# Performance work log

Hardware: AMD Instinct MI355X
Metric: run time of the kernel (lower is better)

Reference implementation:

```python
import jax, jax.numpy as jnp
import numpy as np

EPS = 1e-5
SLOPE = 0.2


def _bn(x, g, b, m, v):
    # eval-mode BatchNorm1d over channel dim (last axis here)
    return (x - m) * (g * jax.lax.rsqrt(v + EPS)) + b


def _lrelu(x):
    return jnp.where(x >= 0, x, SLOPE * x)


def setup_inputs() -> dict:
    key = jax.random.key(0)
    ks = jax.random.split(key, 24)
    B, N = 16, 2048
    d = {
        "x_query": jax.random.normal(ks[0], (B, 2048), jnp.float32),
        "x_key": jax.random.normal(ks[1], (B, N, 512), jnp.float32),
        "W1": jax.random.normal(ks[2], (2048, 512), jnp.float32) * 0.02,
        "W2": jax.random.normal(ks[3], (512, 2048), jnp.float32) * 0.02,
        "W3": jax.random.normal(ks[4], (64, 512), jnp.float32) * 0.02,
        "W4": jax.random.normal(ks[5], (1, 64), jnp.float32) * 0.02,
    }
    for i, c in zip(range(4), (2048, 512, 64, 1)):
        d[f"g{i+1}"] = jax.random.uniform(ks[6 + 4 * i], (c,), jnp.float32, 0.5, 1.5)
        d[f"b{i+1}"] = jax.random.normal(ks[7 + 4 * i], (c,), jnp.float32) * 0.1
        d[f"m{i+1}"] = jax.random.normal(ks[8 + 4 * i], (c,), jnp.float32) * 0.1
        d[f"v{i+1}"] = jax.random.uniform(ks[9 + 4 * i], (c,), jnp.float32, 0.5, 1.5)
    return d


def reference(x_query, x_key, W1, W2, W3, W4,
              g1, b1, m1, v1, g2, b2, m2, v2,
              g3, b3, m3, v3, g4, b4, m4, v4):
    # values: [B, N, 2048]
    values = _lrelu(_bn(jnp.einsum('bnd,ed->bne', x_key, W1), g1, b1, m1, v1))
    features = values + x_query[:, None, :]
    s = _lrelu(_bn(jnp.einsum('bne,de->bnd', features, W2), g2, b2, m2, v2))
    s = _lrelu(_bn(jnp.einsum('bnd,kd->bnk', s, W3), g3, b3, m3, v3))
    s = _lrelu(_bn(jnp.einsum('bnk,ok->bno', s, W4), g4, b4, m4, v4))  # [B,N,1]
    scores = jax.nn.softmax(s[..., 0], axis=1)  # [B,N]
    feature = jnp.einsum('bne,bn->be', values, scores)  # softmax-weighted sum pool
    return feature
```

## Files before the change

kernel.cpp:

```cpp
#include <hip/hip_runtime.h>
#include <hip/hip_bf16.h>

typedef __bf16 bf16x8 __attribute__((ext_vector_type(8)));
typedef float f32x4 __attribute__((ext_vector_type(4)));
typedef __attribute__((address_space(3))) void lds_void_t;
typedef __attribute__((address_space(1))) void gbl_void_t;

#define LRELU(x) ((x) >= 0.f ? (x) : 0.2f * (x))

__device__ __forceinline__ void gload16(void* lds_uniform, const void* gsrc) {
    __builtin_amdgcn_global_load_lds((const gbl_void_t*)gsrc, (lds_void_t*)lds_uniform,
                                     16, 0, 0);
}

__device__ __forceinline__ unsigned short f2u(float f) {
    __hip_bfloat16 h = __float2bfloat16(f);
    return reinterpret_cast<unsigned short&>(h);
}

__global__ void cvt_fused(const float* __restrict__ a, __hip_bfloat16* __restrict__ oa, int na,
                          const float* __restrict__ b, __hip_bfloat16* __restrict__ ob, int nb,
                          const float* __restrict__ c, __hip_bfloat16* __restrict__ oc, int nc,
                          const float* __restrict__ d, __hip_bfloat16* __restrict__ od, int nd) {
    const int stride = gridDim.x * blockDim.x;
    const int total = na + nb + nc + nd;
    for (int i = blockIdx.x * blockDim.x + threadIdx.x; i < total; i += stride) {
        const float* s; __hip_bfloat16* o; int j = i;
        if (j < na) { s = a; o = oa; }
        else {
            j -= na;
            if (j < nb) { s = b; o = ob; }
            else {
                j -= nb;
                if (j < nc) { s = c; o = oc; }
                else { j -= nc; s = d; o = od; }
            }
        }
        float4 v = reinterpret_cast<const float4*>(s)[j];
        ushort4 u;
        u.x = f2u(v.x); u.y = f2u(v.y); u.z = f2u(v.z); u.w = f2u(v.w);
        reinterpret_cast<ushort4*>(o)[j] = u;
    }
}


#define MMQ(AF, BF, IH, JH)                                                   \
    {                                                                         \
        _Pragma("unroll") for (int r = 0; r < 4; ++r) {                       \
            _Pragma("unroll") for (int c = 0; c < 2; ++c) {                   \
                _Pragma("unroll") for (int s = 0; s < 2; ++s) {               \
                    acc[(IH) * 4 + r][(JH) * 2 + c] =                         \
                        __builtin_amdgcn_mfma_f32_16x16x32_bf16(              \
                            AF[r][s], BF[c][s],                               \
                            acc[(IH) * 4 + r][(JH) * 2 + c], 0, 0, 0);        \
                }                                                             \
            }                                                                 \
        }                                                                     \
    }

#define LDA_(AF, BUF, IH)                                                     \
    {                                                                         \
        const __hip_bfloat16* _ab = sm + (BUF) * 32768 + wm * 8192;           \
        _Pragma("unroll") for (int r = 0; r < 4; ++r) {                       \
            const int _row = (IH) * 64 + r * 16 + lr;                         \
            _Pragma("unroll") for (int s = 0; s < 2; ++s) {                   \
                AF[r][s] = *reinterpret_cast<const bf16x8*>(                  \
                    _ab + _row * 64 + (((s * 4 + kg) ^ (lr & 7)) * 8));       \
            }                                                                 \
        }                                                                     \
    }

#define LDB_(BF, BUF, JH)                                                     \
    {                                                                         \
        const __hip_bfloat16* _bb =                                           \
            sm + (BUF) * 32768 + (2 + (wn >> 1)) * 8192;                      \
        _Pragma("unroll") for (int c = 0; c < 2; ++c) {                       \
            const int _row = (wn & 1) * 64 + ((JH) * 2 + c) * 16 + lr;        \
            _Pragma("unroll") for (int s = 0; s < 2; ++s) {                   \
                BF[c][s] = *reinterpret_cast<const bf16x8*>(                  \
                    _bb + _row * 64 + (((s * 4 + kg) ^ (lr & 7)) * 8));       \
            }                                                                 \
        }                                                                     \
    }

#define PH_MID                                                                \
    __builtin_amdgcn_s_barrier();                                             \
    asm volatile("s_waitcnt lgkmcnt(0)" ::: "memory");                        \
    __builtin_amdgcn_sched_barrier(0);                                        \
    __builtin_amdgcn_s_setprio(1);

#define PH_END                                                                \
    __builtin_amdgcn_s_setprio(0);                                            \
    __builtin_amdgcn_sched_barrier(0);                                        \
    __builtin_amdgcn_s_barrier();

template <int N, int K, int MODE>
__global__ __launch_bounds__(512, 1)
void gemm8p(const __hip_bfloat16* __restrict__ A,
            const __hip_bfloat16* __restrict__ Bw,
            const float* __restrict__ xq,
            __hip_bfloat16* __restrict__ out,
            const float* __restrict__ Gg, const float* __restrict__ Gb,
            const float* __restrict__ Gm, const float* __restrict__ Gv) {
    __shared__ __hip_bfloat16 sm[65536];

    const int nwg = gridDim.x;
    const int cpx = nwg >> 3;
    const int bid = blockIdx.x;
    const int orig = (bid & 7) * cpx + (bid >> 3);
    constexpr int NCB = N / 256;
    const int row0 = (orig / NCB) * 256;
    const int col0 = (orig % NCB) * 256;

    const int tid = threadIdx.x;
    const int lane = tid & 63;
    const int wv = tid >> 6;
    const int wm = wv >> 2, wn = wv & 3;
    const int lr = lane & 15, kg = lane >> 4;

    const int schunk = (tid & 7) ^ ((tid >> 3) & 7);
    const __hip_bfloat16* srcA0 = A + (size_t)(row0 + (tid >> 3)) * K + schunk * 8;
    const __hip_bfloat16* srcB0 = Bw + (size_t)(col0 + (tid >> 3)) * K + schunk * 8;
    constexpr size_t H = (size_t)128 * K;

    auto STG = [&](int buf, int region, const __hip_bfloat16* src) {
        __hip_bfloat16* l = sm + buf * 32768 + region * 8192 + wv * 512;
        gload16(l, src);
        gload16(l + 4096, src + (size_t)64 * K);
    };

    f32x4 acc[8][4];
#pragma unroll
    for (int i = 0; i < 8; ++i)
#pragma unroll
        for (int j = 0; j < 4; ++j) acc[i][j] = (f32x4){0.f, 0.f, 0.f, 0.f};

    bf16x8 af[4][2], bfrL[2][2], bfrH[2][2];

    STG(0, 0, srcA0);
    STG(0, 1, srcA0 + H);
    STG(0, 2, srcB0);
    STG(0, 3, srcB0 + H);
    STG(1, 2, srcB0 + 64);
    STG(1, 3, srcB0 + H + 64);
    asm volatile("s_waitcnt vmcnt(4)" ::: "memory");
    __builtin_amdgcn_s_barrier();

    constexpr int niter = K / 128;
    for (int it = 0; it < niter; ++it) {
        const int k0 = it * 128;
        const bool pf = (it + 1 < niter);

        LDA_(af, 0, 0);
        LDB_(bfrL, 0, 0);
        STG(1, 0, srcA0 + k0 + 64);
        PH_MID; MMQ(af, bfrL, 0, 0); PH_END;

        LDB_(bfrH, 0, 1);
        STG(1, 1, srcA0 + H + k0 + 64);
        PH_MID; MMQ(af, bfrH, 0, 1); PH_END;

        LDA_(af, 0, 1);
        if (pf) STG(0, 2, srcB0 + k0 + 128);
        PH_MID; MMQ(af, bfrH, 1, 1); PH_END;

        if (pf) {
            STG(0, 3, srcB0 + H + k0 + 128);
            asm volatile("s_waitcnt vmcnt(4)" ::: "memory");
        } else {
            asm volatile("s_waitcnt vmcnt(0)" ::: "memory");
        }
        PH_MID; MMQ(af, bfrL, 1, 0); PH_END;

        LDA_(af, 1, 0);
        LDB_(bfrL, 1, 0);
        if (pf) STG(0, 0, srcA0 + k0 + 128);
        PH_MID; MMQ(af, bfrL, 0, 0); PH_END;

        LDB_(bfrH, 1, 1);
        if (pf) STG(0, 1, srcA0 + H + k0 + 128);
        PH_MID; MMQ(af, bfrH, 0, 1); PH_END;

        LDA_(af, 1, 1);
        if (pf) STG(1, 2, srcB0 + k0 + 192);
        PH_MID; MMQ(af, bfrH, 1, 1); PH_END;

        if (pf) {
            STG(1, 3, srcB0 + H + k0 + 192);
            asm volatile("s_waitcnt vmcnt(4)" ::: "memory");
        } else {
            asm volatile("s_waitcnt vmcnt(0)" ::: "memory");
        }
        PH_MID; MMQ(af, bfrL, 1, 0); PH_END;
    }

    const int bq = row0 >> 11;
    float scl[4], tcn[4], xqv[4];
#pragma unroll
    for (int j = 0; j < 4; ++j) {
        const int c = col0 + wn * 64 + j * 16 + lr;
        scl[j] = Gg[c] * rsqrtf(Gv[c] + 1e-5f);
        tcn[j] = Gb[c] - Gm[c] * scl[j];
        xqv[j] = (MODE == 1) ? xq[bq * 2048 + c] : 0.f;
    }
#pragma unroll
    for (int i = 0; i < 8; ++i) {
#pragma unroll
        for (int rI = 0; rI < 4; ++rI) {
            const int r = row0 + wm * 128 + i * 16 + kg * 4 + rI;
            const size_t rowoff = (size_t)r * N + col0 + wn * 64 + lr;
#pragma unroll
            for (int j = 0; j < 4; ++j) {
                float val = acc[i][j][rI] * scl[j] + tcn[j];
                val = LRELU(val) + xqv[j];
                out[rowoff + j * 16] = __float2bfloat16(val);
            }
        }
    }
}

__global__ __launch_bounds__(256, 2)
void gemm3_l4(const __hip_bfloat16* __restrict__ A,
              const __hip_bfloat16* __restrict__ W3b,
              const float* __restrict__ W4,
              const float* __restrict__ g3, const float* __restrict__ b3,
              const float* __restrict__ m3, const float* __restrict__ v3,
              const float* __restrict__ g4, const float* __restrict__ b4,
              const float* __restrict__ m4, const float* __restrict__ v4,
              float* __restrict__ logits) {
    __shared__ __hip_bfloat16 lA[128 * 32];
    __shared__ __hip_bfloat16 lB[64 * 520];
    const int tid = threadIdx.x;
    const int lane = tid & 63;
    const int wv = tid >> 6;
    const int row0 = blockIdx.x * 128;
    const int lr = lane & 15, kg = lane >> 4;

#pragma unroll
    for (int p = 0; p < 16; ++p) {
        const int idx = tid * 8 + p * 2048;
        const int r = idx >> 9, c = idx & 511;
        bf16x8 v = *reinterpret_cast<const bf16x8*>(W3b + idx);
        *reinterpret_cast<bf16x8*>(&lB[r * 520 + c]) = v;
    }

    const int schunk = (lane & 3) ^ ((lane >> 3) & 3);
    const __hip_bfloat16* Ag = A + (size_t)(row0 + wv * 32 + (lane >> 2)) * 512 + schunk * 8;
    __hip_bfloat16* lAp = lA + wv * 1024;

    const int koff = ((kg ^ ((lr >> 1) & 3)) << 3);
    const int aoff = (wv * 32 + lr) * 32 + koff;

    f32x4 acc[2][4];
#pragma unroll
    for (int i = 0; i < 2; ++i)
#pragma unroll
        for (int j = 0; j < 4; ++j) acc[i][j] = (f32x4){0.f, 0.f, 0.f, 0.f};

    for (int k = 0; k < 512; k += 32) {
        gload16(lAp,       Ag + k);
        gload16(lAp + 512, Ag + k + (size_t)16 * 512);
        __syncthreads();

        bf16x8 a[2], b[4];
#pragma unroll
        for (int i = 0; i < 2; ++i)
            a[i] = *reinterpret_cast<const bf16x8*>(lA + aoff + i * 512);
#pragma unroll
        for (int j = 0; j < 4; ++j)
            b[j] = *reinterpret_cast<const bf16x8*>(&lB[(j * 16 + lr) * 520 + k + kg * 8]);
#pragma unroll
        for (int i = 0; i < 2; ++i)
#pragma unroll
            for (int j = 0; j < 4; ++j)
                acc[i][j] = __builtin_amdgcn_mfma_f32_16x16x32_bf16(a[i], b[j], acc[i][j], 0, 0, 0);
        __syncthreads();
    }

    const float sc4 = g4[0] * rsqrtf(v4[0] + 1e-5f);
    const float tc4 = b4[0] - m4[0] * sc4;
#pragma unroll
    for (int i = 0; i < 2; ++i) {
        float t[4] = {0.f, 0.f, 0.f, 0.f};
#pragma unroll
        for (int j = 0; j < 4; ++j) {
            const int c = j * 16 + lr;
            const float sc = g3[c] * rsqrtf(v3[c] + 1e-5f);
            const float tc = b3[c] - m3[c] * sc;
            const float w4c = W4[c];
#pragma unroll
            for (int rI = 0; rI < 4; ++rI) {
                float v = acc[i][j][rI] * sc + tc;
                t[rI] += LRELU(v) * w4c;
            }
        }
#pragma unroll
        for (int m = 1; m < 16; m <<= 1)
#pragma unroll
            for (int rI = 0; rI < 4; ++rI) t[rI] += __shfl_xor(t[rI], m, 64);
        if (lr == 0) {
#pragma unroll
            for (int rI = 0; rI < 4; ++rI) {
                float lg = t[rI] * sc4 + tc4;
                logits[row0 + wv * 32 + i * 16 + kg * 4 + rI] = LRELU(lg);
            }
        }
    }
}

__global__ void softmax2048(const float* __restrict__ logits, float* __restrict__ scores) {
    __shared__ float sh[2048];
    __shared__ float red[256];
    const int b = blockIdx.x, tid = threadIdx.x;
    float lmax = -1e30f;
#pragma unroll
    for (int it = 0; it < 8; ++it) {
        const int n = tid + it * 256;
        float v = logits[b * 2048 + n];
        sh[n] = v;
        lmax = fmaxf(lmax, v);
    }
    red[tid] = lmax;
    __syncthreads();
    for (int s = 128; s > 0; s >>= 1) {
        if (tid < s) red[tid] = fmaxf(red[tid], red[tid + s]);
        __syncthreads();
    }
    const float gmax = red[0];
    __syncthreads();
    float lsum = 0.f;
#pragma unroll
    for (int it = 0; it < 8; ++it) {
        const int n = tid + it * 256;
        float e = expf(sh[n] - gmax);
        sh[n] = e;
        lsum += e;
    }
    red[tid] = lsum;
    __syncthreads();
    for (int s = 128; s > 0; s >>= 1) {
        if (tid < s) red[tid] += red[tid + s];
        __syncthreads();
    }
    const float inv = 1.f / red[0];
#pragma unroll
    for (int it = 0; it < 8; ++it) {
        const int n = tid + it * 256;
        scores[b * 2048 + n] = sh[n] * inv;
    }
}

__global__ void pool_partial(const __hip_bfloat16* __restrict__ feats,
                             const float* __restrict__ scores,
                             float* __restrict__ partial) {
    const int b = blockIdx.y, nc = blockIdx.x;
    const int e0 = threadIdx.x * 8;
    float acc[8] = {0, 0, 0, 0, 0, 0, 0, 0};
    const size_t base = ((size_t)b * 2048 + nc * 64) * 2048;
    for (int i = 0; i < 64; ++i) {
        const float sc = scores[b * 2048 + nc * 64 + i];
        bf16x8 v = *reinterpret_cast<const bf16x8*>(feats + base + (size_t)i * 2048 + e0);
#pragma unroll
        for (int j = 0; j < 8; ++j) acc[j] += sc * (float)v[j];
    }
    float* p = partial + ((size_t)(b * 32 + nc)) * 2048 + e0;
#pragma unroll
    for (int j = 0; j < 8; ++j) p[j] = acc[j];
}

__global__ void pool_reduce(const float* __restrict__ partial,
                            const float* __restrict__ xq,
                            float* __restrict__ out) {
    const int i = blockIdx.x * blockDim.x + threadIdx.x;
    const int b = i >> 11, e = i & 2047;
    float s = 0.f;
#pragma unroll
    for (int nc = 0; nc < 32; ++nc) s += partial[((size_t)(b * 32 + nc)) * 2048 + e];
    out[i] = s - xq[i];
}

extern "C" void kernel_launch(void* const* d_in, const int* in_sizes, int n_in,
                              void* d_out, int out_size, void* d_ws, size_t ws_size,
                              hipStream_t stream) {
    const float* xq = (const float*)d_in[0];
    const float* xk = (const float*)d_in[1];
    const float* W1 = (const float*)d_in[2];
    const float* W2 = (const float*)d_in[3];
    const float* W3 = (const float*)d_in[4];
    const float* W4 = (const float*)d_in[5];
    const float* g1 = (const float*)d_in[6], *b1 = (const float*)d_in[7];
    const float* m1 = (const float*)d_in[8], *v1 = (const float*)d_in[9];
    const float* g2 = (const float*)d_in[10], *b2 = (const float*)d_in[11];
    const float* m2 = (const float*)d_in[12], *v2 = (const float*)d_in[13];
    const float* g3 = (const float*)d_in[14], *b3 = (const float*)d_in[15];
    const float* m3 = (const float*)d_in[16], *v3 = (const float*)d_in[17];
    const float* g4 = (const float*)d_in[18], *b4 = (const float*)d_in[19];
    const float* m4 = (const float*)d_in[20], *v4 = (const float*)d_in[21];

    const int M = 32768;

    char* ws = (char*)d_ws;
    size_t off = 0;
    auto alloc = [&](size_t bytes) {
        void* p = ws + off;
        off += (bytes + 255) & ~(size_t)255;
        return p;
    };
    __hip_bfloat16* xkb   = (__hip_bfloat16*)alloc((size_t)M * 512 * 2);
    __hip_bfloat16* w1b   = (__hip_bfloat16*)alloc((size_t)2048 * 512 * 2);
    __hip_bfloat16* w2b   = (__hip_bfloat16*)alloc((size_t)512 * 2048 * 2);
    __hip_bfloat16* w3b   = (__hip_bfloat16*)alloc((size_t)64 * 512 * 2);
    __hip_bfloat16* featb = (__hip_bfloat16*)alloc((size_t)M * 2048 * 2);
    __hip_bfloat16* s2b   = (__hip_bfloat16*)alloc((size_t)M * 512 * 2);
    float* logits         = (float*)alloc((size_t)M * 4);
    float* scores         = (float*)alloc((size_t)16 * 2048 * 4);
    float* partial        = (float*)alloc((size_t)16 * 32 * 2048 * 4);

    cvt_fused<<<4096, 256, 0, stream>>>(
        xk, xkb, M * 512 / 4,
        W1, w1b, 2048 * 512 / 4,
        W2, w2b, 512 * 2048 / 4,
        W3, w3b, 64 * 512 / 4);

    gemm8p<2048, 512, 1><<<1024, 512, 0, stream>>>(
        xkb, w1b, xq, featb, g1, b1, m1, v1);

    gemm8p<512, 2048, 2><<<256, 512, 0, stream>>>(
        featb, w2b, nullptr, s2b, g2, b2, m2, v2);

    gemm3_l4<<<256, 256, 0, stream>>>(s2b, w3b, W4,
                                      g3, b3, m3, v3, g4, b4, m4, v4, logits);

    softmax2048<<<16, 256, 0, stream>>>(logits, scores);

    pool_partial<<<dim3(32, 16), 256, 0, stream>>>(featb, scores, partial);
    pool_reduce<<<128, 256, 0, stream>>>(partial, xq, (float*)d_out);
}
```

Measured before the change: 205.1 us.

## Fuse x_key fp32-to-bf16 conversion into first GEMM's A-tile loader

Drops the separate pass that converted x_key (32768x512 fp32) to a bf16 buffer. The first GEMM now reads fp32 A tiles straight into registers, converts them to bf16 and writes them to LDS, with register double-buffering woven into the existing pipelined schedule. This removes a full read and write of the converted activation buffer. In exchange the first GEMM reads twice as many bytes for A, uses more VGPRs, and loses async direct-to-LDS loads for A.

```diff
diff --git a/kernel.cpp b/kernel.cpp
--- a/kernel.cpp
+++ b/kernel.cpp
@@ -18,23 +18,18 @@
     return reinterpret_cast<unsigned short&>(h);
 }
 
-__global__ void cvt_fused(const float* __restrict__ a, __hip_bfloat16* __restrict__ oa, int na,
-                          const float* __restrict__ b, __hip_bfloat16* __restrict__ ob, int nb,
-                          const float* __restrict__ c, __hip_bfloat16* __restrict__ oc, int nc,
-                          const float* __restrict__ d, __hip_bfloat16* __restrict__ od, int nd) {
+__global__ void cvt_w(const float* __restrict__ a, __hip_bfloat16* __restrict__ oa, int na,
+                      const float* __restrict__ b, __hip_bfloat16* __restrict__ ob, int nb,
+                      const float* __restrict__ c, __hip_bfloat16* __restrict__ oc, int nc) {
     const int stride = gridDim.x * blockDim.x;
-    const int total = na + nb + nc + nd;
+    const int total = na + nb + nc;
     for (int i = blockIdx.x * blockDim.x + threadIdx.x; i < total; i += stride) {
         const float* s; __hip_bfloat16* o; int j = i;
         if (j < na) { s = a; o = oa; }
         else {
             j -= na;
             if (j < nb) { s = b; o = ob; }
-            else {
-                j -= nb;
-                if (j < nc) { s = c; o = oc; }
-                else { j -= nc; s = d; o = od; }
-            }
+            else { j -= nb; s = c; o = oc; }
         }
         float4 v = reinterpret_cast<const float4*>(s)[j];
         ushort4 u;
@@ -94,9 +89,10 @@
     __builtin_amdgcn_sched_barrier(0);                                        \
     __builtin_amdgcn_s_barrier();
 
-template <int N, int K, int MODE>
+template <int N, int K, int MODE, int ASRC>
 __global__ __launch_bounds__(512, 1)
 void gemm8p(const __hip_bfloat16* __restrict__ A,
+            const float* __restrict__ Af,
             const __hip_bfloat16* __restrict__ Bw,
             const float* __restrict__ xq,
             __hip_bfloat16* __restrict__ out,
@@ -120,6 +116,7 @@
 
     const int schunk = (tid & 7) ^ ((tid >> 3) & 7);
     const __hip_bfloat16* srcA0 = A + (size_t)(row0 + (tid >> 3)) * K + schunk * 8;
+    const float* srcAf = Af + (size_t)(row0 + (tid >> 3)) * K + schunk * 8;
     const __hip_bfloat16* srcB0 = Bw + (size_t)(col0 + (tid >> 3)) * K + schunk * 8;
     constexpr size_t H = (size_t)128 * K;
 
@@ -128,6 +125,26 @@
         gload16(l, src);
         gload16(l + 4096, src + (size_t)64 * K);
     };
+    auto LD_A32 = [&](float4* r, int elemoff) {
+#pragma unroll
+        for (int g = 0; g < 2; ++g) {
+            const float* s = srcAf + elemoff + g * (size_t)64 * K;
+            r[g * 2 + 0] = *reinterpret_cast<const float4*>(s);
+            r[g * 2 + 1] = *reinterpret_cast<const float4*>(s + 4);
+        }
+    };
+    auto WR_A32 = [&](int buf, int region, const float4* r) {
+        __hip_bfloat16* l = sm + buf * 32768 + region * 8192 + tid * 8;
+#pragma unroll
+        for (int g = 0; g < 2; ++g) {
+            bf16x8 v;
+            v[0] = (__bf16)r[g * 2].x;     v[1] = (__bf16)r[g * 2].y;
+            v[2] = (__bf16)r[g * 2].z;     v[3] = (__bf16)r[g * 2].w;
+            v[4] = (__bf16)r[g * 2 + 1].x; v[5] = (__bf16)r[g * 2 + 1].y;
+            v[6] = (__bf16)r[g * 2 + 1].z; v[7] = (__bf16)r[g * 2 + 1].w;
+            *reinterpret_cast<bf16x8*>(l + g * 4096) = v;
+        }
+    };
 
     f32x4 acc[8][4];
 #pragma unroll
@@ -136,14 +153,28 @@
         for (int j = 0; j < 4; ++j) acc[i][j] = (f32x4){0.f, 0.f, 0.f, 0.f};
 
     bf16x8 af[4][2], bfrL[2][2], bfrH[2][2];
-
-    STG(0, 0, srcA0);
-    STG(0, 1, srcA0 + H);
-    STG(0, 2, srcB0);
-    STG(0, 3, srcB0 + H);
-    STG(1, 2, srcB0 + 64);
-    STG(1, 3, srcB0 + H + 64);
-    asm volatile("s_waitcnt vmcnt(4)" ::: "memory");
+    float4 rE0[4], rE1[4], rO0[4], rO1[4];
+
+    if constexpr (ASRC == 1) {
+        float4 t0[4], t1[4];
+        LD_A32(t0, 0); LD_A32(t1, (int)H);
+        STG(0, 2, srcB0);
+        STG(0, 3, srcB0 + H);
+        STG(1, 2, srcB0 + 64);
+        STG(1, 3, srcB0 + H + 64);
+        LD_A32(rO0, 64); LD_A32(rO1, (int)H + 64);
+        WR_A32(0, 0, t0); WR_A32(0, 1, t1);
+        asm volatile("s_waitcnt vmcnt(12)" ::: "memory");
+        asm volatile("s_waitcnt lgkmcnt(0)" ::: "memory");
+    } else {
+        STG(0, 0, srcA0);
+        STG(0, 1, srcA0 + H);
+        STG(0, 2, srcB0);
+        STG(0, 3, srcB0 + H);
+        STG(1, 2, srcB0 + 64);
+        STG(1, 3, srcB0 + H + 64);
+        asm volatile("s_waitcnt vmcnt(4)" ::: "memory");
+    }
     __builtin_amdgcn_s_barrier();
 
     constexpr int niter = K / 128;
@@ -151,13 +182,23 @@
         const int k0 = it * 128;
         const bool pf = (it + 1 < niter);
 
+        if constexpr (ASRC == 1) {
+            if (pf) LD_A32(rE0, k0 + 128);
+            WR_A32(1, 0, rO0);
+        } else {
+            STG(1, 0, srcA0 + k0 + 64);
+        }
         LDA_(af, 0, 0);
         LDB_(bfrL, 0, 0);
-        STG(1, 0, srcA0 + k0 + 64);
         PH_MID; MMQ(af, bfrL, 0, 0); PH_END;
 
+        if constexpr (ASRC == 1) {
+            if (pf) LD_A32(rE1, (int)H + k0 + 128);
+            WR_A32(1, 1, rO1);
+        } else {
+            STG(1, 1, srcA0 + H + k0 + 64);
+        }
         LDB_(bfrH, 0, 1);
-        STG(1, 1, srcA0 + H + k0 + 64);
         PH_MID; MMQ(af, bfrH, 0, 1); PH_END;
 
         LDA_(af, 0, 1);
@@ -166,7 +207,10 @@
 
         if (pf) {
             STG(0, 3, srcB0 + H + k0 + 128);
-            asm volatile("s_waitcnt vmcnt(4)" ::: "memory");
+            if constexpr (ASRC == 1)
+                asm volatile("s_waitcnt vmcnt(12)" ::: "memory");
+            else
+                asm volatile("s_waitcnt vmcnt(4)" ::: "memory");
         } else {
             asm volatile("s_waitcnt vmcnt(0)" ::: "memory");
         }
@@ -174,11 +218,19 @@
 
         LDA_(af, 1, 0);
         LDB_(bfrL, 1, 0);
-        if (pf) STG(0, 0, srcA0 + k0 + 128);
+        if constexpr (ASRC == 1) {
+            if (pf) { LD_A32(rO0, k0 + 192); WR_A32(0, 0, rE0); }
+        } else {
+            if (pf) STG(0, 0, srcA0 + k0 + 128);
+        }
         PH_MID; MMQ(af, bfrL, 0, 0); PH_END;
 
         LDB_(bfrH, 1, 1);
-        if (pf) STG(0, 1, srcA0 + H + k0 + 128);
+        if constexpr (ASRC == 1) {
+            if (pf) { LD_A32(rO1, (int)H + k0 + 192); WR_A32(0, 1, rE1); }
+        } else {
+            if (pf) STG(0, 1, srcA0 + H + k0 + 128);
+        }
         PH_MID; MMQ(af, bfrH, 0, 1); PH_END;
 
         LDA_(af, 1, 1);
@@ -187,7 +239,10 @@
 
         if (pf) {
             STG(1, 3, srcB0 + H + k0 + 192);
-            asm volatile("s_waitcnt vmcnt(4)" ::: "memory");
+            if constexpr (ASRC == 1)
+                asm volatile("s_waitcnt vmcnt(12)" ::: "memory");
+            else
+                asm volatile("s_waitcnt vmcnt(4)" ::: "memory");
         } else {
             asm volatile("s_waitcnt vmcnt(0)" ::: "memory");
         }
@@ -406,7 +461,6 @@
         off += (bytes + 255) & ~(size_t)255;
         return p;
     };
-    __hip_bfloat16* xkb   = (__hip_bfloat16*)alloc((size_t)M * 512 * 2);
     __hip_bfloat16* w1b   = (__hip_bfloat16*)alloc((size_t)2048 * 512 * 2);
     __hip_bfloat16* w2b   = (__hip_bfloat16*)alloc((size_t)512 * 2048 * 2);
     __hip_bfloat16* w3b   = (__hip_bfloat16*)alloc((size_t)64 * 512 * 2);
@@ -416,17 +470,16 @@
     float* scores         = (float*)alloc((size_t)16 * 2048 * 4);
     float* partial        = (float*)alloc((size_t)16 * 32 * 2048 * 4);
 
-    cvt_fused<<<4096, 256, 0, stream>>>(
-        xk, xkb, M * 512 / 4,
+    cvt_w<<<512, 256, 0, stream>>>(
         W1, w1b, 2048 * 512 / 4,
         W2, w2b, 512 * 2048 / 4,
         W3, w3b, 64 * 512 / 4);
 
-    gemm8p<2048, 512, 1><<<1024, 512, 0, stream>>>(
-        xkb, w1b, xq, featb, g1, b1, m1, v1);
-
-    gemm8p<512, 2048, 2><<<256, 512, 0, stream>>>(
-        featb, w2b, nullptr, s2b, g2, b2, m2, v2);
+    gemm8p<2048, 512, 1, 1><<<1024, 512, 0, stream>>>(
+        nullptr, xk, w1b, xq, featb, g1, b1, m1, v1);
+
+    gemm8p<512, 2048, 2, 0><<<256, 512, 0, stream>>>(
+        featb, nullptr, w2b, nullptr, s2b, g2, b2, m2, v2);
 
     gemm3_l4<<<256, 256, 0, stream>>>(s2b, w3b, W4,
                                       g3, b3, m3, v3, g4, b4, m4, v4, logits);
```

Measured after the change: 300.8 us. +46.7%, slower.
